# Performance work log

Hardware: AMD Instinct MI355X
Metric: run time of the kernel (lower is better)

Reference implementation:

```python
import jax, jax.numpy as jnp
import numpy as np
from jax import lax

B, C, T, S = 32, 122, 500, 13
WID, EMB, PROJ = 80, 8, 1024
HID = 768  # (H=1)*(W=96)*(E=8) after CNN
EPS = 1e-5
DN = ('NCHW', 'OIHW', 'NCHW')


def setup_inputs() -> dict:
    key = jax.random.key(0)
    ks = jax.random.split(key, 24)
    f32 = jnp.float32
    def n(k, shape, scale):
        return (jax.random.normal(k, shape, dtype=f32) * scale).astype(f32)
    return {
        'x': jax.random.normal(ks[0], (B, C, T), dtype=f32),
        'subject_ids': jax.random.randint(ks[1], (B,), 0, S, dtype=jnp.int32),
        'W_sub': n(ks[2], (S, T, T), 0.04),      # nn.Linear(500,500) weight per subject
        'b_sub': n(ks[3], (S, T), 0.02),
        'conv1_w': n(ks[4], (WID, 1, 1, 5), 0.3),
        'conv1_b': n(ks[5], (WID,), 0.02),
        'bn1_g': 1.0 + n(ks[6], (WID,), 0.1),
        'bn1_b': n(ks[7], (WID,), 0.1),
        'bn1_m': n(ks[8], (WID,), 0.1),
        'bn1_v': 0.5 + jax.random.uniform(ks[9], (WID,), dtype=f32),
        'conv2_w': n(ks[10], (WID, WID, C, 1), 0.01),
        'conv2_b': n(ks[11], (WID,), 0.02),
        'bn2_g': 1.0 + n(ks[12], (WID,), 0.1),
        'bn2_b': n(ks[13], (WID,), 0.1),
        'bn2_m': n(ks[14], (WID,), 0.1),
        'bn2_v': 0.5 + jax.random.uniform(ks[15], (WID,), dtype=f32),
        'proj_w': n(ks[16], (EMB, WID, 1, 1), 0.1),
        'proj_b': n(ks[17], (EMB,), 0.02),
        'mlp1_w': n(ks[18], (PROJ, HID), 0.03),
        'mlp1_b': n(ks[19], (PROJ,), 0.02),
        'mlp2_w': n(ks[20], (PROJ, PROJ), 0.03),
        'mlp2_b': n(ks[21], (PROJ,), 0.02),
        'ln_g': 1.0 + n(ks[22], (PROJ,), 0.05),
        'ln_b': n(ks[23], (PROJ,), 0.05),
    }


def _bn(h, g, b, m, v):
    # eval-mode BatchNorm2d over channel axis 1
    scale = (g / jnp.sqrt(v + EPS))[None, :, None, None]
    shift = (b - m * g / jnp.sqrt(v + EPS))[None, :, None, None]
    return h * scale + shift


def _forward(x, subject_ids, W_sub, b_sub, conv1_w, conv1_b, bn1_g, bn1_b, bn1_m, bn1_v,
             conv2_w, conv2_b, bn2_g, bn2_b, bn2_m, bn2_v, proj_w, proj_b,
             mlp1_w, mlp1_b, mlp2_w, mlp2_b, ln_g, ln_b):
    # --- per-subject routing: gather each sample's Linear(500,500) and apply ---
    Wg = W_sub[subject_ids]                       # [B,T,T] (out,in)
    bg = b_sub[subject_ids]                       # [B,T]
    out = jnp.einsum('bcs,bts->bct', x, Wg) + bg[:, None, :]
    # --- spatio-temporal CNN (eval mode: dropout = identity) ---
    h = out[:, None, :, :]                        # [B,1,C,T]
    h = lax.conv_general_dilated(h, conv1_w, (1, 1), 'VALID', dimension_numbers=DN)
    h = h + conv1_b[None, :, None, None]          # [B,80,122,496]
    h = lax.reduce_window(h, 0.0, lax.add, (1, 1, 1, 17), (1, 1, 1, 5), 'VALID') / 17.0  # [B,80,122,96]
    h = jax.nn.elu(_bn(h, bn1_g, bn1_b, bn1_m, bn1_v))
    h = lax.conv_general_dilated(h, conv2_w, (1, 1), 'VALID', dimension_numbers=DN)
    h = h + conv2_b[None, :, None, None]          # [B,80,1,96]
    h = jax.nn.elu(_bn(h, bn2_g, bn2_b, bn2_m, bn2_v))
    h = lax.conv_general_dilated(h, proj_w, (1, 1), 'VALID', dimension_numbers=DN)
    h = h + proj_b[None, :, None, None]           # [B,8,1,96]
    z = jnp.transpose(h, (0, 2, 3, 1)).reshape(h.shape[0], -1)  # [B,768]
    # --- MLP projector: Linear -> Residual(GELU+Linear) -> LayerNorm ---
    z1 = z @ mlp1_w.T + mlp1_b                    # [B,1024]
    r = jax.nn.gelu(z1, approximate=False) @ mlp2_w.T + mlp2_b
    y = z1 + r
    mu = jnp.mean(y, axis=-1, keepdims=True)
    var = jnp.var(y, axis=-1, keepdims=True)
    return (y - mu) / jnp.sqrt(var + EPS) * ln_g + ln_b


def reference(x, subject_ids, W_sub, b_sub, conv1_w, conv1_b, bn1_g, bn1_b, bn1_m, bn1_v,
              conv2_w, conv2_b, bn2_g, bn2_b, bn2_m, bn2_v, proj_w, proj_b,
              mlp1_w, mlp1_b, mlp2_w, mlp2_b, ln_g, ln_b):
    return _forward(x, subject_ids, W_sub, b_sub, conv1_w, conv1_b, bn1_g, bn1_b, bn1_m, bn1_v,
                    conv2_w, conv2_b, bn2_g, bn2_b, bn2_m, bn2_v, proj_w, proj_b,
                    mlp1_w, mlp1_b, mlp2_w, mlp2_b, ln_g, ln_b)
```

## Files before the change

kernel.cpp:

```cpp
#include <hip/hip_runtime.h>
#include <math.h>

#define BB 32
#define CC 122
#define TT 500
#define SS 13
#define WID 80
#define EMB 8
#define PROJ 1024
#define HID 768
#define TP 96
#define EPSF 1e-5f
#define KP 9760
#define KSPLIT 16

typedef float f32x4 __attribute__((ext_vector_type(4)));
typedef __bf16 bf16x8 __attribute__((ext_vector_type(8)));
typedef unsigned short u16x8 __attribute__((ext_vector_type(8)));
union BF8 { u16x8 u; bf16x8 b; };

__device__ __forceinline__ unsigned short f2bf(float f) {
    union { float f; unsigned u; } v; v.f = f;
    unsigned r = v.u + 0x7FFFu + ((v.u >> 16) & 1u);
    return (unsigned short)(r >> 16);
}

__device__ __forceinline__ float eluf(float x) {
    return x > 0.f ? x : __expf(x) - 1.f;
}

#define OFF_E    ((size_t)0)
#define OFF_XB   ((size_t)1952000)
#define OFF_W2P  ((size_t)4704512)
#define OFF_PART ((size_t)20086272)
#define OFF_Z    ((size_t)24018432)
#define OFF_Z1   ((size_t)24030720)
#define OFF_G    ((size_t)24063488)
#define OFF_Y    ((size_t)24079872)
#define OFF_W1B  ((size_t)24112640)
#define OFF_W2B  ((size_t)24505856)
#define OFF_WCB  ((size_t)25030144)
#define OFF_B1F  ((size_t)25031424)
#define OFF_SC2  ((size_t)25031504)
#define OFF_SH2  ((size_t)25031584)

#define NPK_X  (2097152)
#define NPK_W2 (780800)
#define NPK_M1 (786432)
#define NPK_M2 (1048576)
#define NPK_TOT (NPK_X + NPK_W2 + NPK_M1 + NPK_M2)

__global__ __launch_bounds__(256) void k_pack(const float* __restrict__ x,
                                              const float* __restrict__ conv2_w,
                                              const float* __restrict__ mlp1_w,
                                              const float* __restrict__ mlp2_w,
                                              const float* __restrict__ conv1_w, const float* __restrict__ conv1_b,
                                              const float* __restrict__ g1, const float* __restrict__ b1,
                                              const float* __restrict__ m1, const float* __restrict__ v1,
                                              const float* __restrict__ conv2_b, const float* __restrict__ g2,
                                              const float* __restrict__ b2, const float* __restrict__ m2,
                                              const float* __restrict__ v2,
                                              unsigned short* __restrict__ xb,
                                              unsigned short* __restrict__ w2p,
                                              unsigned short* __restrict__ w1b,
                                              unsigned short* __restrict__ w2b,
                                              unsigned short* __restrict__ wcb, float* __restrict__ bias1f,
                                              float* __restrict__ scale2, float* __restrict__ shift2f) {
    if (blockIdx.x == 0) {
        int o = threadIdx.x;
        if (o < WID) {
            float s1 = g1[o] * rsqrtf(v1[o] + EPSF);
            float sh1 = b1[o] - m1[o] * s1;
            #pragma unroll
            for (int d = 0; d < 21; d++) {
                int klo = d - 16; if (klo < 0) klo = 0;
                int khi = d;      if (khi > 4) khi = 4;
                float acc = 0.f;
                for (int k = klo; k <= khi; k++) acc += conv1_w[o*5 + k];
                wcb[o*32 + d] = f2bf(acc * s1 * (1.f/17.f));
            }
            #pragma unroll
            for (int d = 21; d < 32; d++) wcb[o*32 + d] = 0;
            bias1f[o] = conv1_b[o] * s1 + sh1;
            float s2 = g2[o] * rsqrtf(v2[o] + EPSF);
            scale2[o] = s2;
            shift2f[o] = conv2_b[o] * s2 + (b2[o] - m2[o] * s2);
        }
    }
    size_t idx = (size_t)blockIdx.x * 256 + threadIdx.x;
    if (idx >= (size_t)NPK_TOT) return;
    if (idx < NPK_X) {
        int s = idx & 511, c = (idx >> 9) & 127, b = idx >> 16;
        float v = (c < CC && s < TT) ? x[((size_t)b * CC + c) * TT + s] : 0.f;
        xb[idx] = f2bf(v);
    } else if (idx < NPK_X + NPK_W2) {
        size_t j = idx - NPK_X;
        int o  = (int)(j / (WID * CC));
        int r  = (int)(j % (WID * CC));
        int op = r / CC, c = r % CC;
        w2p[(size_t)o * KP + (size_t)c * WID + op] = f2bf(conv2_w[j]);
    } else if (idx < NPK_X + NPK_W2 + NPK_M1) {
        size_t j = idx - NPK_X - NPK_W2;
        w1b[j] = f2bf(mlp1_w[j]);
    } else {
        size_t j = idx - NPK_X - NPK_W2 - NPK_M1;
        w2b[j] = f2bf(mlp2_w[j]);
    }
}

__global__ __launch_bounds__(256) void k_einsum(const unsigned short* __restrict__ xb,
                                                const float* __restrict__ W_sub,
                                                const int* __restrict__ sid,
                                                const float* __restrict__ b_sub,
                                                unsigned short* __restrict__ oute) {
    __shared__ unsigned short bt[32 * 520];
    int t0 = blockIdx.x * 32, b = blockIdx.y;
    int s = sid[b];
    int tid = threadIdx.x, w = tid >> 6, lr = tid & 15, lg = (tid >> 4) & 3;
    {
        const float* src = W_sub + (size_t)s * (TT * TT);
        for (int i = tid; i < 2048; i += 256) {
            int row = i >> 6;
            int c0  = (i & 63) << 3;
            int rt  = t0 + row;
            union { unsigned short h[8]; uint4 q; } pk;
            if (rt < TT && c0 + 8 <= TT) {
                const float* p = src + (size_t)rt * TT + c0;
                float4 v0 = *(const float4*)p;
                float4 v1 = *(const float4*)(p + 4);
                pk.h[0] = f2bf(v0.x); pk.h[1] = f2bf(v0.y);
                pk.h[2] = f2bf(v0.z); pk.h[3] = f2bf(v0.w);
                pk.h[4] = f2bf(v1.x); pk.h[5] = f2bf(v1.y);
                pk.h[6] = f2bf(v1.z); pk.h[7] = f2bf(v1.w);
            } else {
                const float* p = src + (size_t)rt * TT;
                #pragma unroll
                for (int j = 0; j < 8; j++)
                    pk.h[j] = (rt < TT && c0 + j < TT) ? f2bf(p[c0 + j]) : (unsigned short)0;
            }
            *(uint4*)(&bt[row * 520 + c0]) = pk.q;
        }
    }
    __syncthreads();
    const unsigned short* A0 = xb + ((size_t)(b * 128 + w * 32 + lr)) * 512 + 8 * lg;
    f32x4 acc[2][2] = {};
    for (int kb = 0; kb < 512; kb += 32) {
        BF8 a0, a1;
        a0.u = *(const u16x8*)(A0 + kb);
        a1.u = *(const u16x8*)(A0 + 16 * 512 + kb);
        #pragma unroll
        for (int nt = 0; nt < 2; nt++) {
            BF8 bf; bf.u = *(const u16x8*)(bt + (nt * 16 + lr) * 520 + kb + 8 * lg);
            acc[0][nt] = __builtin_amdgcn_mfma_f32_16x16x32_bf16(a0.b, bf.b, acc[0][nt], 0, 0, 0);
            acc[1][nt] = __builtin_amdgcn_mfma_f32_16x16x32_bf16(a1.b, bf.b, acc[1][nt], 0, 0, 0);
        }
    }
    const float* bg = b_sub + (size_t)s * TT;
    #pragma unroll
    for (int nt = 0; nt < 2; nt++) {
        int t = t0 + nt * 16 + lr;
        if (t < TT) {
            float bias = bg[t];
            #pragma unroll
            for (int mt = 0; mt < 2; mt++) {
                int crow = w * 32 + mt * 16 + 4 * lg;
                #pragma unroll
                for (int r = 0; r < 4; r++) {
                    int c = crow + r;
                    if (c < CC) oute[((size_t)b * CC + c) * TT + t] = f2bf(acc[mt][nt][r] + bias);
                }
            }
        }
    }
}

__global__ __launch_bounds__(384) void k_fc(const unsigned short* __restrict__ oute,
                                            const unsigned short* __restrict__ wcb,
                                            const float* __restrict__ b1f,
                                            const unsigned short* __restrict__ w2p,
                                            float* __restrict__ part) {
    __shared__ unsigned short e2[2][512];
    __shared__ unsigned short pt[96][164];
    int chunk = blockIdx.x, b = blockIdx.y;
    int tid = threadIdx.x, w = tid >> 6, l = tid & 63, lr = l & 15, lg = l >> 4;
    BF8 af[5]; float4 bf4[5];
    #pragma unroll
    for (int ot = 0; ot < 5; ot++) {
        af[ot].u = *(const u16x8*)(wcb + (ot * 16 + lr) * 32 + 8 * lg);
        bf4[ot] = *(const float4*)(b1f + ot * 16 + 4 * lg);
    }
    const unsigned short* Arow = w2p + (size_t)lr * KP + 8 * lg;
    f32x4 acc2[5] = {};
    for (int ci = 0; ci < 4; ci++) {
        int cp = chunk * 4 + ci;
        bool live = cp < 61;
        if (live) {
            if (tid < 250) {
                int cc = tid / 125, i = tid % 125;
                ((uint2*)e2[cc])[i] = ((const uint2*)(oute + ((size_t)b * CC + cp * 2 + cc) * TT))[i];
            }
            if (tid >= 232 && tid < 256) {
                int j = tid - 232; int cc = j / 12, i = 500 + (j % 12);
                e2[cc][i] = 0;
            }
        }
        __syncthreads();
        if (live) {
            #pragma unroll
            for (int cc = 0; cc < 2; cc++) {
                int t = w * 16 + lr;
                const unsigned short* ew = e2[cc] + 5 * t + 8 * lg;
                BF8 bfr;
                #pragma unroll
                for (int j = 0; j < 8; j++) bfr.u[j] = ew[j];
                f32x4 fa[5] = {};
                #pragma unroll
                for (int ot = 0; ot < 5; ot++)
                    fa[ot] = __builtin_amdgcn_mfma_f32_16x16x32_bf16(af[ot].b, bfr.b, fa[ot], 0, 0, 0);
                #pragma unroll
                for (int ot = 0; ot < 5; ot++) {
                    union { unsigned short s[4]; uint2 v; } pk;
                    #pragma unroll
                    for (int r = 0; r < 4; r++) pk.s[r] = f2bf(eluf(fa[ot][r] + bf4[ot][r]));
                    *(uint2*)&pt[t][cc * 80 + ot * 16 + 4 * lg] = pk.v;
                }
            }
        }
        __syncthreads();
        if (live) {
            #pragma unroll
            for (int kl = 0; kl < 5; kl++) {
                BF8 bf; bf.u = *(const u16x8*)(&pt[w * 16 + lr][kl * 32 + lg * 8]);
                int ko = cp * 160 + kl * 32;
                #pragma unroll
                for (int mt = 0; mt < 5; mt++) {
                    BF8 a; a.u = *(const u16x8*)(Arow + (size_t)mt * 16 * KP + ko);
                    acc2[mt] = __builtin_amdgcn_mfma_f32_16x16x32_bf16(a.b, bf.b, acc2[mt], 0, 0, 0);
                }
            }
        }
    }
    float* pp = part + ((size_t)(chunk * BB + b) * WID) * TP;
    int t = w * 16 + lr;
    #pragma unroll
    for (int mt = 0; mt < 5; mt++) {
        int ob = mt * 16 + 4 * lg;
        #pragma unroll
        for (int r = 0; r < 4; r++)
            pp[(size_t)(ob + r) * TP + t] = acc2[mt][r];
    }
}

__global__ __launch_bounds__(256) void k_redproj(const float* __restrict__ part,
                                                 const float* __restrict__ scale2,
                                                 const float* __restrict__ shift2f,
                                                 const float* __restrict__ pw,
                                                 const float* __restrict__ pb,
                                                 unsigned short* __restrict__ zbf) {
    __shared__ float ly[WID * 12];
    __shared__ float lw[EMB * WID];
    int tq = blockIdx.x, b = blockIdx.y;
    int tid = threadIdx.x;
    int t0 = tq * 12;
    for (int i = tid; i < EMB * WID; i += 256) lw[i] = pw[i];
    if (tid < 240) {
        int o = tid / 3, q = tid % 3;
        const float* pbase = part + (size_t)b * (WID * TP) + o * TP + t0 + 4 * q;
        float4 a = {0.f, 0.f, 0.f, 0.f};
        #pragma unroll
        for (int ks = 0; ks < KSPLIT; ks++) {
            float4 v = *(const float4*)(pbase + (size_t)ks * (BB * WID * TP));
            a.x += v.x; a.y += v.y; a.z += v.z; a.w += v.w;
        }
        float sc = scale2[o], sh = shift2f[o];
        ly[o * 12 + 4 * q + 0] = eluf(a.x * sc + sh);
        ly[o * 12 + 4 * q + 1] = eluf(a.y * sc + sh);
        ly[o * 12 + 4 * q + 2] = eluf(a.z * sc + sh);
        ly[o * 12 + 4 * q + 3] = eluf(a.w * sc + sh);
    }
    __syncthreads();
    if (tid < 12 * EMB) {
        int e = tid & 7, tl = tid >> 3;
        float acc = pb[e];
        #pragma unroll 10
        for (int o = 0; o < WID; o++) acc = fmaf(ly[o * 12 + tl], lw[e * WID + o], acc);
        zbf[(size_t)b * HID + (t0 + tl) * EMB + e] = f2bf(acc);
    }
}

__global__ __launch_bounds__(256) void k_mlp1(const unsigned short* __restrict__ zbf,
                                              const unsigned short* __restrict__ w1b,
                                              const float* __restrict__ bias,
                                              float* __restrict__ z1,
                                              unsigned short* __restrict__ gbf) {
    __shared__ float accb[4][64][4];
    int cu = blockIdx.x >> 1, rh = blockIdx.x & 1;
    int tid = threadIdx.x, w = tid >> 6, l = tid & 63, lr = l & 15, lg = l >> 4;
    int pcol = cu * 16 + lr;
    const unsigned short* wr = w1b + (size_t)pcol * HID + w * 192 + 8 * lg;
    const unsigned short* za = zbf + (size_t)(rh * 16 + lr) * HID + w * 192 + 8 * lg;
    f32x4 acc = {};
    #pragma unroll
    for (int kb = 0; kb < 192; kb += 32) {
        BF8 bf; bf.u = *(const u16x8*)(wr + kb);
        BF8 a;  a.u  = *(const u16x8*)(za + kb);
        acc = __builtin_amdgcn_mfma_f32_16x16x32_bf16(a.b, bf.b, acc, 0, 0, 0);
    }
    #pragma unroll
    for (int r = 0; r < 4; r++) accb[w][l][r] = acc[r];
    __syncthreads();
    if (w == 0) {
        float bs = bias[pcol];
        #pragma unroll
        for (int r = 0; r < 4; r++) {
            int row = rh * 16 + 4 * lg + r;
            float v = bs;
            #pragma unroll
            for (int q = 0; q < 4; q++) v += accb[q][l][r];
            z1[(size_t)row * PROJ + pcol] = v;
            gbf[(size_t)row * PROJ + pcol] = f2bf(0.5f * v * (1.f + erff(v * 0.70710678118654752f)));
        }
    }
}

__global__ __launch_bounds__(256) void k_mlp2(const unsigned short* __restrict__ gbf,
                                              const float* __restrict__ z1,
                                              const unsigned short* __restrict__ w2b,
                                              const float* __restrict__ bias,
                                              float* __restrict__ y) {
    __shared__ float accb[4][64][4];
    int cu = blockIdx.x >> 1, rh = blockIdx.x & 1;
    int tid = threadIdx.x, w = tid >> 6, l = tid & 63, lr = l & 15, lg = l >> 4;
    int pc = cu * 16 + lr;
    const unsigned short* wr = w2b + (size_t)pc * PROJ + w * 256 + 8 * lg;
    const unsigned short* ga = gbf + (size_t)(rh * 16 + lr) * PROJ + w * 256 + 8 * lg;
    f32x4 acc = {};
    #pragma unroll
    for (int kb = 0; kb < 256; kb += 32) {
        BF8 bf; bf.u = *(const u16x8*)(wr + kb);
        BF8 a;  a.u  = *(const u16x8*)(ga + kb);
        acc = __builtin_amdgcn_mfma_f32_16x16x32_bf16(a.b, bf.b, acc, 0, 0, 0);
    }
    #pragma unroll
    for (int r = 0; r < 4; r++) accb[w][l][r] = acc[r];
    __syncthreads();
    if (w == 0) {
        float bs = bias[pc];
        #pragma unroll
        for (int r = 0; r < 4; r++) {
            int row = rh * 16 + 4 * lg + r;
            float v = bs + z1[(size_t)row * PROJ + pc];
            #pragma unroll
            for (int q = 0; q < 4; q++) v += accb[q][l][r];
            y[(size_t)row * PROJ + pc] = v;
        }
    }
}

__global__ __launch_bounds__(256) void k_ln(const float* __restrict__ y,
                                            const float* __restrict__ lg,
                                            const float* __restrict__ lb,
                                            float* __restrict__ out) {
    int b = blockIdx.x, tid = threadIdx.x;
    const float4* yr = (const float4*)(y + (size_t)b * PROJ);
    float4 v = yr[tid];
    float s  = v.x + v.y + v.z + v.w;
    float sq = v.x*v.x + v.y*v.y + v.z*v.z + v.w*v.w;
    #pragma unroll
    for (int off = 32; off > 0; off >>= 1) {
        s  += __shfl_down(s, off);
        sq += __shfl_down(sq, off);
    }
    __shared__ float ss[4], ssq[4];
    int wv = tid >> 6, lane = tid & 63;
    if (lane == 0) { ss[wv] = s; ssq[wv] = sq; }
    __syncthreads();
    __shared__ float smu, sinv;
    if (tid == 0) {
        float Sm = ss[0] + ss[1] + ss[2] + ss[3];
        float Sq = ssq[0] + ssq[1] + ssq[2] + ssq[3];
        float mu = Sm * (1.f / PROJ);
        float var = Sq * (1.f / PROJ) - mu * mu;
        smu = mu;
        sinv = rsqrtf(var + EPSF);
    }
    __syncthreads();
    float mu = smu, inv = sinv;
    float4 g4 = ((const float4*)lg)[tid];
    float4 b4 = ((const float4*)lb)[tid];
    float4 o4;
    o4.x = (v.x - mu) * inv * g4.x + b4.x;
    o4.y = (v.y - mu) * inv * g4.y + b4.y;
    o4.z = (v.z - mu) * inv * g4.z + b4.z;
    o4.w = (v.w - mu) * inv * g4.w + b4.w;
    ((float4*)(out + (size_t)b * PROJ))[tid] = o4;
}

extern "C" void kernel_launch(void* const* d_in, const int* in_sizes, int n_in,
                              void* d_out, int out_size, void* d_ws, size_t ws_size,
                              hipStream_t stream) {
    const float* x        = (const float*)d_in[0];
    const int*   sid      = (const int*)  d_in[1];
    const float* W_sub    = (const float*)d_in[2];
    const float* b_sub    = (const float*)d_in[3];
    const float* conv1_w  = (const float*)d_in[4];
    const float* conv1_b  = (const float*)d_in[5];
    const float* bn1_g    = (const float*)d_in[6];
    const float* bn1_b    = (const float*)d_in[7];
    const float* bn1_m    = (const float*)d_in[8];
    const float* bn1_v    = (const float*)d_in[9];
    const float* conv2_w  = (const float*)d_in[10];
    const float* conv2_b  = (const float*)d_in[11];
    const float* bn2_g    = (const float*)d_in[12];
    const float* bn2_b    = (const float*)d_in[13];
    const float* bn2_m    = (const float*)d_in[14];
    const float* bn2_v    = (const float*)d_in[15];
    const float* proj_w   = (const float*)d_in[16];
    const float* proj_b   = (const float*)d_in[17];
    const float* mlp1_w   = (const float*)d_in[18];
    const float* mlp1_b   = (const float*)d_in[19];
    const float* mlp2_w   = (const float*)d_in[20];
    const float* mlp2_b   = (const float*)d_in[21];
    const float* ln_g     = (const float*)d_in[22];
    const float* ln_b     = (const float*)d_in[23];
    float* out = (float*)d_out;
    float* ws  = (float*)d_ws;

    unsigned short* ws_e   = (unsigned short*)(ws + OFF_E);
    unsigned short* ws_xb  = (unsigned short*)(ws + OFF_XB);
    unsigned short* ws_w2p = (unsigned short*)(ws + OFF_W2P);
    float* ws_part = ws + OFF_PART;
    unsigned short* ws_zbf = (unsigned short*)(ws + OFF_Z);
    float* ws_z1   = ws + OFF_Z1;
    unsigned short* ws_gbf = (unsigned short*)(ws + OFF_G);
    float* ws_y    = ws + OFF_Y;
    unsigned short* ws_w1b = (unsigned short*)(ws + OFF_W1B);
    unsigned short* ws_w2b = (unsigned short*)(ws + OFF_W2B);
    unsigned short* ws_wcb = (unsigned short*)(ws + OFF_WCB);
    float* ws_b1f  = ws + OFF_B1F;
    float* ws_sc2  = ws + OFF_SC2;
    float* ws_sh2  = ws + OFF_SH2;

    hipLaunchKernelGGL(k_pack, dim3((NPK_TOT + 255) / 256), dim3(256), 0, stream,
                       x, conv2_w, mlp1_w, mlp2_w,
                       conv1_w, conv1_b, bn1_g, bn1_b, bn1_m, bn1_v,
                       conv2_b, bn2_g, bn2_b, bn2_m, bn2_v,
                       ws_xb, ws_w2p, ws_w1b, ws_w2b,
                       ws_wcb, ws_b1f, ws_sc2, ws_sh2);

    hipLaunchKernelGGL(k_einsum, dim3(16, BB), dim3(256), 0, stream,
                       ws_xb, W_sub, sid, b_sub, ws_e);

    hipLaunchKernelGGL(k_fc, dim3(KSPLIT, BB), dim3(384), 0, stream,
                       ws_e, ws_wcb, ws_b1f, ws_w2p, ws_part);

    hipLaunchKernelGGL(k_redproj, dim3(8, BB), dim3(256), 0, stream,
                       ws_part, ws_sc2, ws_sh2, proj_w, proj_b, ws_zbf);

    hipLaunchKernelGGL(k_mlp1, dim3(128), dim3(256), 0, stream,
                       ws_zbf, ws_w1b, mlp1_b, ws_z1, ws_gbf);

    hipLaunchKernelGGL(k_mlp2, dim3(128), dim3(256), 0, stream,
                       ws_gbf, ws_z1, ws_w2b, mlp2_b, ws_y);

    hipLaunchKernelGGL(k_ln, dim3(BB), dim3(256), 0, stream,
                       ws_y, ln_g, ln_b, out);
}
```

Baseline: 199.3 us.

## Transpose conv2 weights via LDS in pack and stage A-tiles in LDS for k_fc

The pack kernel now gives one block to each conv2 output channel. Each block transposes that channel's weights through shared memory, so the global stores are coalesced 16-byte writes instead of scattered 2-byte writes. In k_fc, each 80x160 weight slice is now loaded cooperatively into LDS once per chunk, instead of every wave reading the A fragments from global memory separately. This adds a barrier per iteration and about 27KB of LDS, which may lower occupancy of k_fc.

```diff
diff --git a/kernel.cpp b/kernel.cpp
--- a/kernel.cpp
+++ b/kernel.cpp
@@ -45,10 +45,9 @@
 #define OFF_SH2  ((size_t)25031584)
 
 #define NPK_X  (2097152)
-#define NPK_W2 (780800)
 #define NPK_M1 (786432)
 #define NPK_M2 (1048576)
-#define NPK_TOT (NPK_X + NPK_W2 + NPK_M1 + NPK_M2)
+#define NPK_LIN (NPK_X + NPK_M1 + NPK_M2)
 
 __global__ __launch_bounds__(256) void k_pack(const float* __restrict__ x,
                                               const float* __restrict__ conv2_w,
@@ -66,9 +65,11 @@
                                               unsigned short* __restrict__ w2b,
                                               unsigned short* __restrict__ wcb, float* __restrict__ bias1f,
                                               float* __restrict__ scale2, float* __restrict__ shift2f) {
-    if (blockIdx.x == 0) {
-        int o = threadIdx.x;
-        if (o < WID) {
+    __shared__ unsigned short lt[WID][124];
+    int bid = blockIdx.x, tid = threadIdx.x;
+    if (bid < WID) {
+        if (bid == 0 && tid < WID) {
+            int o = tid;
             float s1 = g1[o] * rsqrtf(v1[o] + EPSF);
             float sh1 = b1[o] - m1[o] * s1;
             #pragma unroll
@@ -86,24 +87,37 @@
             scale2[o] = s2;
             shift2f[o] = conv2_b[o] * s2 + (b2[o] - m2[o] * s2);
         }
-    }
-    size_t idx = (size_t)blockIdx.x * 256 + threadIdx.x;
-    if (idx >= (size_t)NPK_TOT) return;
+        int o = bid;
+        const float* src = conv2_w + (size_t)o * (WID * CC);
+        for (int i = tid; i < WID * CC; i += 256) {
+            int op = i / CC, c = i - op * CC;
+            lt[op][c] = f2bf(src[i]);
+        }
+        __syncthreads();
+        unsigned short* dst = w2p + (size_t)o * KP;
+        for (int j = tid; j < KP / 8; j += 256) {
+            int k0 = j * 8;
+            union { unsigned short h[8]; uint4 q; } pk;
+            #pragma unroll
+            for (int u = 0; u < 8; u++) {
+                int k = k0 + u;
+                pk.h[u] = lt[k % WID][k / WID];
+            }
+            *(uint4*)(dst + k0) = pk.q;
+        }
+        return;
+    }
+    size_t idx = (size_t)(bid - WID) * 256 + tid;
+    if (idx >= (size_t)NPK_LIN) return;
     if (idx < NPK_X) {
         int s = idx & 511, c = (idx >> 9) & 127, b = idx >> 16;
         float v = (c < CC && s < TT) ? x[((size_t)b * CC + c) * TT + s] : 0.f;
         xb[idx] = f2bf(v);
-    } else if (idx < NPK_X + NPK_W2) {
+    } else if (idx < NPK_X + NPK_M1) {
         size_t j = idx - NPK_X;
-        int o  = (int)(j / (WID * CC));
-        int r  = (int)(j % (WID * CC));
-        int op = r / CC, c = r % CC;
-        w2p[(size_t)o * KP + (size_t)c * WID + op] = f2bf(conv2_w[j]);
-    } else if (idx < NPK_X + NPK_W2 + NPK_M1) {
-        size_t j = idx - NPK_X - NPK_W2;
         w1b[j] = f2bf(mlp1_w[j]);
     } else {
-        size_t j = idx - NPK_X - NPK_W2 - NPK_M1;
+        size_t j = idx - NPK_X - NPK_M1;
         w2b[j] = f2bf(mlp2_w[j]);
     }
 }
@@ -181,6 +195,7 @@
                                             float* __restrict__ part) {
     __shared__ unsigned short e2[2][512];
     __shared__ unsigned short pt[96][164];
+    __shared__ unsigned short aw[WID][168];
     int chunk = blockIdx.x, b = blockIdx.y;
     int tid = threadIdx.x, w = tid >> 6, l = tid & 63, lr = l & 15, lg = l >> 4;
     BF8 af[5]; float4 bf4[5];
@@ -189,11 +204,11 @@
         af[ot].u = *(const u16x8*)(wcb + (ot * 16 + lr) * 32 + 8 * lg);
         bf4[ot] = *(const float4*)(b1f + ot * 16 + 4 * lg);
     }
-    const unsigned short* Arow = w2p + (size_t)lr * KP + 8 * lg;
     f32x4 acc2[5] = {};
     for (int ci = 0; ci < 4; ci++) {
         int cp = chunk * 4 + ci;
         bool live = cp < 61;
+        __syncthreads();
         if (live) {
             if (tid < 250) {
                 int cc = tid / 125, i = tid % 125;
@@ -202,6 +217,11 @@
             if (tid >= 232 && tid < 256) {
                 int j = tid - 232; int cc = j / 12, i = 500 + (j % 12);
                 e2[cc][i] = 0;
+            }
+            const unsigned short* wsrc = w2p + (size_t)cp * 160;
+            for (int i = tid; i < WID * 20; i += 384) {
+                int o = i / 20, c8 = i - o * 20;
+                *(u16x8*)(&aw[o][c8 * 8]) = *(const u16x8*)(wsrc + (size_t)o * KP + c8 * 8);
             }
         }
         __syncthreads();
@@ -231,10 +251,9 @@
             #pragma unroll
             for (int kl = 0; kl < 5; kl++) {
                 BF8 bf; bf.u = *(const u16x8*)(&pt[w * 16 + lr][kl * 32 + lg * 8]);
-                int ko = cp * 160 + kl * 32;
                 #pragma unroll
                 for (int mt = 0; mt < 5; mt++) {
-                    BF8 a; a.u = *(const u16x8*)(Arow + (size_t)mt * 16 * KP + ko);
+                    BF8 a; a.u = *(const u16x8*)(&aw[mt * 16 + lr][kl * 32 + lg * 8]);
                     acc2[mt] = __builtin_amdgcn_mfma_f32_16x16x32_bf16(a.b, bf.b, acc2[mt], 0, 0, 0);
                 }
             }
@@ -441,7 +460,7 @@
     float* ws_sc2  = ws + OFF_SC2;
     float* ws_sh2  = ws + OFF_SH2;
 
-    hipLaunchKernelGGL(k_pack, dim3((NPK_TOT + 255) / 256), dim3(256), 0, stream,
+    hipLaunchKernelGGL(k_pack, dim3(WID + (NPK_LIN + 255) / 256), dim3(256), 0, stream,
                        x, conv2_w, mlp1_w, mlp2_w,
                        conv1_w, conv1_b, bn1_g, bn1_b, bn1_m, bn1_v,
                        conv2_b, bn2_g, bn2_b, bn2_m, bn2_v,
```

New measurement: 195.3 us. 2.0% less time.
